# Kernel optimization log

Hardware: AMD Instinct MI355X
Metric: run time of the kernel (lower is better)

Reference implementation:

```python
import jax, jax.numpy as jnp
import numpy as np

B, TED, G, N, E, MD, NOISE = 10000, 512, 64, 2000, 64000, 15, 128
PAC = 10
PACDIM = (TED + NOISE) * PAC  # 6400
D0, D1 = 1024, 512


def _linear_params(k, fan_in, fan_out):
    kw, kb = jax.random.split(k)
    lim = 1.0 / np.sqrt(fan_in)
    w = jax.random.uniform(kw, (fan_in, fan_out), minval=-lim, maxval=lim, dtype=jnp.float32)
    b = jax.random.uniform(kb, (fan_out,), minval=-lim, maxval=lim, dtype=jnp.float32)
    return w, b


def setup_inputs() -> dict:
    key = jax.random.key(0)
    ks = jax.random.split(key, 12)
    inp = {
        'input_': jax.random.normal(ks[0], (B, TED), dtype=jnp.float32),
        'graphs_x': jax.random.normal(ks[1], (G, N, 1), dtype=jnp.float32),
        'edge_index': jax.random.randint(ks[2], (G, 2, E), 0, N, dtype=jnp.int32),
        'graph_ids': jax.random.randint(ks[3], (B,), 0, G, dtype=jnp.int32),
        'chain': jax.random.normal(ks[4], (B, 1), dtype=jnp.float32),
        'metadata': jax.random.normal(ks[5], (B, MD), dtype=jnp.float32),
    }
    inp['gcn_w'], inp['gcn_b'] = _linear_params(ks[6], 1, 1)
    inp['meta_w'], inp['meta_b'] = _linear_params(ks[7], 1 + MD, 32)
    inp['gme_w'], inp['gme_b'] = _linear_params(ks[8], N + 32, NOISE)
    inp['seq_w0'], inp['seq_b0'] = _linear_params(ks[9], PACDIM, D0)
    inp['seq_w1'], inp['seq_b1'] = _linear_params(ks[10], D0, D1)
    inp['seq_w2'], inp['seq_b2'] = _linear_params(ks[11], D1, 1)
    return inp


def _gcn_one(x, ei, gcn_w, gcn_b):
    # GCNConv(1,1) with self-loops and symmetric normalization.
    loops = jnp.arange(N, dtype=ei.dtype)
    src = jnp.concatenate([ei[0], loops])
    dst = jnp.concatenate([ei[1], loops])
    deg = jax.ops.segment_sum(jnp.ones_like(src, dtype=x.dtype), dst, num_segments=N)
    dinv = jax.lax.rsqrt(deg)  # deg >= 1 due to self-loops
    norm = dinv[src] * dinv[dst]  # [E+N]
    xw = x @ gcn_w  # [N,1]
    msg = xw[src] * norm[:, None]
    out = jax.ops.segment_sum(msg, dst, num_segments=N) + gcn_b
    return out.reshape(-1)  # flatten -> [N]


def reference(input_, graphs_x, edge_index, graph_ids, chain, metadata,
              gcn_w, gcn_b, meta_w, meta_b, gme_w, gme_b,
              seq_w0, seq_b0, seq_w1, seq_b1, seq_w2, seq_b2):
    # per-unique-graph GCN, vectorized over G graphs
    gcn_out = jax.vmap(lambda x, ei: _gcn_one(x, ei, gcn_w, gcn_b))(graphs_x, edge_index)  # [G,N]
    graph_emb = gcn_out[graph_ids]  # gather: [B,N]
    all_meta = jnp.concatenate([chain, metadata], axis=1)  # [B,1+MD]
    meta_emb = jax.nn.relu(all_meta @ meta_w + meta_b)  # [B,32]
    noise = jnp.concatenate([graph_emb, meta_emb], axis=1) @ gme_w + gme_b  # [B,NOISE]
    h = jnp.concatenate([input_, noise], axis=1).reshape(-1, PACDIM)  # [B/PAC, PACDIM]
    h = jax.nn.leaky_relu(h @ seq_w0 + seq_b0, 0.2)  # dropout omitted (eval mode)
    h = jax.nn.leaky_relu(h @ seq_w1 + seq_b1, 0.2)
    return h @ seq_w2 + seq_b2  # [B/PAC, 1]
```

## Files before the change

kernel.cpp:

```cpp
#include <hip/hip_runtime.h>

typedef __bf16 bf16_t;
typedef __bf16 bf16x4 __attribute__((ext_vector_type(4)));
typedef __bf16 bf16x8 __attribute__((ext_vector_type(8)));
typedef float floatx4 __attribute__((ext_vector_type(4)));

#define G_GRAPHS 64
#define N_NODES 2000
#define N_EDGES 64000
#define BATCH 10000
#define TED_ 512
#define NOISE_ 128
#define PACDIM_ 6400
#define D0_ 1024
#define D1_ 512
#define MROWS 1000
#define ESPLIT 8
#define EPB (N_EDGES / ESPLIT)
#define S0 8
#define S1 8

__device__ __forceinline__ void glds16(const void* g, void* l) {
    __builtin_amdgcn_global_load_lds(
        (__attribute__((address_space(1))) void*)(g),
        (__attribute__((address_space(3))) void*)(l), 16, 0, 0);
}

__global__ __launch_bounds__(256) void zero_kernel(float4* __restrict__ p, int n4) {
    int i = blockIdx.x * 256 + threadIdx.x;
    if (i < n4) p[i] = make_float4(0.f, 0.f, 0.f, 0.f);
}

__global__ __launch_bounds__(512) void deg_kernel(
    const int* __restrict__ edge_index, float* __restrict__ degs)
{
    __shared__ float h[N_NODES];
    const int g = blockIdx.y, s = blockIdx.x, tid = threadIdx.x;
    for (int n = tid; n < N_NODES; n += 512) h[n] = 0.f;
    __syncthreads();
    const int* dst = edge_index + (size_t)g * 2 * N_EDGES + N_EDGES + s * EPB;
    for (int e = tid; e < EPB; e += 512) atomicAdd(&h[dst[e]], 1.0f);
    __syncthreads();
    float* dg = degs + (size_t)g * N_NODES;
    for (int n = tid; n < N_NODES; n += 512) {
        float v = h[n];
        if (v != 0.f) atomicAdd(&dg[n], v);
    }
}

__global__ __launch_bounds__(512) void msg_kernel(
    const float* __restrict__ graphs_x, const int* __restrict__ edge_index,
    const float* __restrict__ degs, float* __restrict__ outs)
{
    __shared__ float xsl[N_NODES];
    __shared__ float dvl[N_NODES];
    __shared__ float oh[N_NODES];
    const int g = blockIdx.y, s = blockIdx.x, tid = threadIdx.x;
    const float* xg = graphs_x + (size_t)g * N_NODES;
    const float* dgg = degs + (size_t)g * N_NODES;
    for (int n = tid; n < N_NODES; n += 512) {
        xsl[n] = xg[n];
        dvl[n] = rsqrtf(dgg[n] + 1.0f);
        oh[n] = 0.f;
    }
    __syncthreads();
    const int* src = edge_index + (size_t)g * 2 * N_EDGES + s * EPB;
    const int* dst = src + N_EDGES;
    for (int e = tid; e < EPB; e += 512) {
        int ss = src[e], dd = dst[e];
        atomicAdd(&oh[dd], xsl[ss] * dvl[ss] * dvl[dd]);
    }
    __syncthreads();
    float* og = outs + (size_t)g * N_NODES;
    for (int n = tid; n < N_NODES; n += 512) {
        float v = oh[n];
        if (v != 0.f) atomicAdd(&og[n], v);
    }
}

__global__ __launch_bounds__(512) void gnoise_part_kernel(
    const float* __restrict__ graphs_x, const float* __restrict__ degs,
    const float* __restrict__ outs,
    const float* __restrict__ gcn_w, const float* __restrict__ gcn_b,
    const float* __restrict__ gme_w, float* __restrict__ gnoise)
{
    __shared__ float of[500];
    __shared__ float part[4][128];
    const int s = blockIdx.x, g = blockIdx.y, tid = threadIdx.x;
    const int nBase = s * 500;
    const float w = gcn_w[0], b = gcn_b[0];
    for (int n = tid; n < 500; n += 512) {
        int gn = nBase + n;
        float di2 = 1.0f / (degs[(size_t)g * N_NODES + gn] + 1.0f);
        of[n] = w * (outs[(size_t)g * N_NODES + gn]
                     + graphs_x[(size_t)g * N_NODES + gn] * di2) + b;
    }
    __syncthreads();
    const int j = tid & 127, ch = tid >> 7;
    float acc = 0.f;
    const int n0 = ch * 125;
    for (int n = n0; n < n0 + 125; n++)
        acc += of[n] * gme_w[(size_t)(nBase + n) * 128 + j];
    part[ch][j] = acc;
    __syncthreads();
    if (tid < 128)
        atomicAdd(&gnoise[(size_t)g * 128 + tid],
                  part[0][tid] + part[1][tid] + part[2][tid] + part[3][tid]);
}

__global__ __launch_bounds__(256) void pack_meta_kernel(
    const float* __restrict__ in,
    const float* __restrict__ chain, const float* __restrict__ metadata,
    const int* __restrict__ graph_ids,
    const float* __restrict__ meta_w, const float* __restrict__ meta_b,
    const float* __restrict__ gme_w, const float* __restrict__ gme_b,
    const float* __restrict__ gnoise, bf16_t* __restrict__ A)
{
    if (blockIdx.x < 5000) {
        int idx = blockIdx.x * 256 + threadIdx.x;
        float4 v = ((const float4*)in)[idx];
        int b = idx >> 7;
        int c = (idx & 127) << 2;
        int r = b / 10, slot = b - r * 10;
        bf16x4 o = { (bf16_t)v.x, (bf16_t)v.y, (bf16_t)v.z, (bf16_t)v.w };
        *(bf16x4*)(A + (size_t)r * PACDIM_ + slot * 640 + c) = o;
        return;
    }
    int wid = ((blockIdx.x - 5000) * 256 + threadIdx.x) >> 6;
    int lane = threadIdx.x & 63;
    if (wid >= BATCH) return;
    const int b = wid;
    float me = 0.f;
    if (lane < 32) {
        me = meta_b[lane] + chain[b] * meta_w[lane];
        for (int i = 1; i < 16; i++)
            me += metadata[(size_t)b * 15 + (i - 1)] * meta_w[(size_t)i * 32 + lane];
        me = me > 0.f ? me : 0.f;
    }
    const int gid = graph_ids[b];
    const int j1 = lane, j2 = lane + 64;
    float n1 = gnoise[(size_t)gid * 128 + j1] + gme_b[j1];
    float n2 = gnoise[(size_t)gid * 128 + j2] + gme_b[j2];
    for (int k = 0; k < 32; k++) {
        float mk = __shfl(me, k, 64);
        const float* wrow = gme_w + (size_t)(N_NODES + k) * 128;
        n1 += mk * wrow[j1];
        n2 += mk * wrow[j2];
    }
    int r = b / 10, slot = b - r * 10;
    bf16_t* dp = A + (size_t)r * PACDIM_ + slot * 640 + TED_;
    dp[j1] = (bf16_t)n1;
    dp[j2] = (bf16_t)n2;
}

__global__ __launch_bounds__(256) void transpose_bf16_kernel(
    const float* __restrict__ W, bf16_t* __restrict__ Wt, int R, int C)
{
    __shared__ float t[32][33];
    int c0 = blockIdx.x * 32, r0 = blockIdx.y * 32;
    int tx = threadIdx.x & 31, ty = threadIdx.x >> 5;
    for (int yy = ty; yy < 32; yy += 8)
        t[yy][tx] = W[(size_t)(r0 + yy) * C + c0 + tx];
    __syncthreads();
    for (int yy = ty; yy < 32; yy += 8)
        Wt[(size_t)(c0 + yy) * R + r0 + tx] = (bf16_t)t[tx][yy];
}

__global__ __launch_bounds__(256) void gemm_bt_splitk_kernel(
    const bf16_t* __restrict__ A,
    const bf16_t* __restrict__ Bt,
    float* __restrict__ P,
    int M, int N, int K, int KS)
{
    __shared__ __align__(16) bf16_t As[128 * 32];
    __shared__ __align__(16) bf16_t Bs[128 * 32];
    const int tid = threadIdx.x;
    const int wave = tid >> 6;
    const int lane = tid & 63;
    const int mBase = blockIdx.y * 128;
    const int nBase = blockIdx.x * 128;
    const int z = blockIdx.z;
    const int Mp = gridDim.y * 128;
    const int wm = (wave & 1) * 64;
    const int wn = (wave >> 1) * 64;

    floatx4 acc[4][4] = {};

    const int c0 = tid, c1 = tid + 256;
    const int rA0 = c0 >> 2, k80 = (c0 & 3) * 8;
    const int rA1 = c1 >> 2, k81 = (c1 & 3) * 8;
    int gm0 = mBase + rA0; if (gm0 > M - 1) gm0 = M - 1;
    int gm1 = mBase + rA1; if (gm1 > M - 1) gm1 = M - 1;
    const bf16_t* aP0 = A + (size_t)gm0 * K + k80;
    const bf16_t* aP1 = A + (size_t)gm1 * K + k81;
    const bf16_t* bP0 = Bt + (size_t)(nBase + rA0) * K + k80;
    const bf16_t* bP1 = Bt + (size_t)(nBase + rA1) * K + k81;
    char* lA0 = (char*)As + wave * 1024;
    char* lA1 = (char*)As + 4096 + wave * 1024;
    char* lB0 = (char*)Bs + wave * 1024;
    char* lB1 = (char*)Bs + 4096 + wave * 1024;

    const int kq = (lane >> 4) * 8;
    const int mr = lane & 15;
    const bf16x8* ra[4]; const bf16x8* rb[4];
    for (int i = 0; i < 4; i++)
        ra[i] = (const bf16x8*)&As[(wm + i * 16 + mr) * 32 + kq];
    for (int j = 0; j < 4; j++)
        rb[j] = (const bf16x8*)&Bs[(wn + j * 16 + mr) * 32 + kq];

    const int kEnd = z * KS + KS;
    for (int k0 = z * KS; k0 < kEnd; k0 += 32) {
        __syncthreads();
        glds16(aP0 + k0, lA0);
        glds16(aP1 + k0, lA1);
        glds16(bP0 + k0, lB0);
        glds16(bP1 + k0, lB1);
        __syncthreads();
        bf16x8 af[4], bfr[4];
        for (int i = 0; i < 4; i++) af[i] = *ra[i];
        for (int j = 0; j < 4; j++) bfr[j] = *rb[j];
        for (int i = 0; i < 4; i++)
            for (int j = 0; j < 4; j++)
                acc[i][j] = __builtin_amdgcn_mfma_f32_16x16x32_bf16(
                    af[i], bfr[j], acc[i][j], 0, 0, 0);
    }

    float* Pz = P + (size_t)z * Mp * N;
    const int rq = (lane >> 4) * 4;
    const int cn = lane & 15;
    for (int j = 0; j < 4; j++) {
        int col = nBase + wn + j * 16 + cn;
        for (int i = 0; i < 4; i++)
            for (int r = 0; r < 4; r++) {
                int rowm = mBase + wm + i * 16 + rq + r;
                Pz[(size_t)rowm * N + col] = acc[i][j][r];
            }
    }
}

__global__ __launch_bounds__(256) void reduce_bias_leaky_kernel(
    const float* __restrict__ P, const float* __restrict__ bias,
    bf16_t* __restrict__ C, int M, int N, int Mp, int S)
{
    int idx = blockIdx.x * 256 + threadIdx.x;
    int total = M * (N >> 2);
    if (idx >= total) return;
    int nv = N >> 2;
    int r = idx / nv, c4 = (idx - r * nv) << 2;
    size_t off = (size_t)r * N + c4;
    size_t stride = (size_t)Mp * N;
    float4 v = *(const float4*)(P + off);
    for (int s = 1; s < S; s++) {
        float4 u = *(const float4*)(P + s * stride + off);
        v.x += u.x; v.y += u.y; v.z += u.z; v.w += u.w;
    }
    const float4 bv = *(const float4*)(bias + c4);
    v.x += bv.x; v.y += bv.y; v.z += bv.z; v.w += bv.w;
    v.x = v.x > 0.f ? v.x : 0.2f * v.x;
    v.y = v.y > 0.f ? v.y : 0.2f * v.y;
    v.z = v.z > 0.f ? v.z : 0.2f * v.z;
    v.w = v.w > 0.f ? v.w : 0.2f * v.w;
    bf16x4 o = { (bf16_t)v.x, (bf16_t)v.y, (bf16_t)v.z, (bf16_t)v.w };
    *(bf16x4*)(C + off) = o;
}

__global__ __launch_bounds__(256) void final_fused_kernel(
    const float* __restrict__ P, const float* __restrict__ b1,
    const float* __restrict__ w2, const float* __restrict__ b2,
    float* __restrict__ out, int Mp, int S)
{
    int wid = (blockIdx.x * 256 + threadIdx.x) >> 6;
    int lane = threadIdx.x & 63;
    if (wid >= MROWS) return;
    size_t stride = (size_t)Mp * D1_;
    const float* base = P + (size_t)wid * D1_;
    float s = 0.f;
    for (int i = 0; i < 8; i++) {
        int c = i * 64 + lane;
        float v = base[c];
        for (int z = 1; z < S; z++) v += base[(size_t)z * stride + c];
        v += b1[c];
        v = v > 0.f ? v : 0.2f * v;
        s += v * w2[c];
    }
    for (int off = 32; off; off >>= 1) s += __shfl_down(s, off, 64);
    if (lane == 0) out[wid] = s + b2[0];
}

extern "C" void kernel_launch(void* const* d_in, const int* in_sizes, int n_in,
                              void* d_out, int out_size, void* d_ws, size_t ws_size,
                              hipStream_t stream)
{
    const float* input_    = (const float*)d_in[0];
    const float* graphs_x  = (const float*)d_in[1];
    const int*   edge_idx  = (const int*)  d_in[2];
    const int*   graph_ids = (const int*)  d_in[3];
    const float* chain     = (const float*)d_in[4];
    const float* metadata  = (const float*)d_in[5];
    const float* gcn_w     = (const float*)d_in[6];
    const float* gcn_b     = (const float*)d_in[7];
    const float* meta_w    = (const float*)d_in[8];
    const float* meta_b    = (const float*)d_in[9];
    const float* gme_w     = (const float*)d_in[10];
    const float* gme_b     = (const float*)d_in[11];
    const float* seq_w0    = (const float*)d_in[12];
    const float* seq_b0    = (const float*)d_in[13];
    const float* seq_w1    = (const float*)d_in[14];
    const float* seq_b1    = (const float*)d_in[15];
    const float* seq_w2    = (const float*)d_in[16];
    const float* seq_b2    = (const float*)d_in[17];
    float* out = (float*)d_out;

    char* ws = (char*)d_ws;
    float*  gnoise = (float*)(ws + 0);
    float*  degs   = (float*)(ws + 32768);
    float*  outs   = (float*)(ws + 544768);
    bf16_t* Abuf   = (bf16_t*)(ws + 1056768);
    bf16_t* W0t    = (bf16_t*)(ws + 13856768);
    bf16_t* W1t    = (bf16_t*)(ws + 26963968);
    bf16_t* H1     = (bf16_t*)(ws + 28012544);
    float*  P      = (float*)(ws + 30060544);

    const int zn4 = (32768 + 512000 + 512000) / 16;
    zero_kernel<<<(zn4 + 255) / 256, 256, 0, stream>>>((float4*)gnoise, zn4);
    deg_kernel<<<dim3(ESPLIT, G_GRAPHS), 512, 0, stream>>>(edge_idx, degs);
    msg_kernel<<<dim3(ESPLIT, G_GRAPHS), 512, 0, stream>>>(graphs_x, edge_idx, degs, outs);
    gnoise_part_kernel<<<dim3(4, G_GRAPHS), 512, 0, stream>>>(
        graphs_x, degs, outs, gcn_w, gcn_b, gme_w, gnoise);

    pack_meta_kernel<<<7500, 256, 0, stream>>>(
        input_, chain, metadata, graph_ids, meta_w, meta_b, gme_w, gme_b,
        gnoise, Abuf);
    transpose_bf16_kernel<<<dim3(D0_ / 32, PACDIM_ / 32), 256, 0, stream>>>(
        seq_w0, W0t, PACDIM_, D0_);
    transpose_bf16_kernel<<<dim3(D1_ / 32, D0_ / 32), 256, 0, stream>>>(
        seq_w1, W1t, D0_, D1_);

    gemm_bt_splitk_kernel<<<dim3(D0_ / 128, 8, S0), 256, 0, stream>>>(
        Abuf, W0t, P, MROWS, D0_, PACDIM_, PACDIM_ / S0);
    reduce_bias_leaky_kernel<<<(MROWS * D0_ / 4 + 255) / 256, 256, 0, stream>>>(
        P, seq_b0, H1, MROWS, D0_, 1024, S0);

    gemm_bt_splitk_kernel<<<dim3(D1_ / 128, 8, S1), 256, 0, stream>>>(
        H1, W1t, P, MROWS, D1_, D0_, D0_ / S1);
    final_fused_kernel<<<(MROWS * 64 + 255) / 256, 256, 0, stream>>>(
        P, seq_b1, seq_w2, seq_b2, out, 1024, S1);
}
```

Baseline: 279.0 us.

## Fuse prep kernels, replace global atomics with partial buffers, double-buffer GEMM LDS

Merges the degree histogram, input packing and both weight transposes into one prep kernel, which removes the zero kernel and several launches. Per-split degree and message results are now written to partial buffers and summed by the consumers instead of being accumulated with global atomics. The split-K GEMM gains double-buffered LDS so the next K tile loads while the current one is being multiplied, with one barrier per iteration. The cost is more workspace and extra partial-sum reads in the downstream kernels.

```diff
diff --git a/kernel.cpp b/kernel.cpp
--- a/kernel.cpp
+++ b/kernel.cpp
@@ -26,41 +26,69 @@
         (__attribute__((address_space(3))) void*)(l), 16, 0, 0);
 }
 
-__global__ __launch_bounds__(256) void zero_kernel(float4* __restrict__ p, int n4) {
-    int i = blockIdx.x * 256 + threadIdx.x;
-    if (i < n4) p[i] = make_float4(0.f, 0.f, 0.f, 0.f);
-}
-
-__global__ __launch_bounds__(512) void deg_kernel(
-    const int* __restrict__ edge_index, float* __restrict__ degs)
+__global__ __launch_bounds__(256) void prep_kernel(
+    const int* __restrict__ edge_index, float* __restrict__ degs_part,
+    const float* __restrict__ in, bf16_t* __restrict__ A,
+    const float* __restrict__ W0, bf16_t* __restrict__ W0t,
+    const float* __restrict__ W1, bf16_t* __restrict__ W1t)
 {
     __shared__ float h[N_NODES];
-    const int g = blockIdx.y, s = blockIdx.x, tid = threadIdx.x;
-    for (int n = tid; n < N_NODES; n += 512) h[n] = 0.f;
-    __syncthreads();
-    const int* dst = edge_index + (size_t)g * 2 * N_EDGES + N_EDGES + s * EPB;
-    for (int e = tid; e < EPB; e += 512) atomicAdd(&h[dst[e]], 1.0f);
-    __syncthreads();
-    float* dg = degs + (size_t)g * N_NODES;
-    for (int n = tid; n < N_NODES; n += 512) {
-        float v = h[n];
-        if (v != 0.f) atomicAdd(&dg[n], v);
-    }
+    __shared__ float t[32][33];
+    const int b = blockIdx.x, tid = threadIdx.x;
+    if (b < 512) {
+        const int s = b & 7, g = b >> 3;
+        for (int n = tid; n < N_NODES; n += 256) h[n] = 0.f;
+        __syncthreads();
+        const int* dst = edge_index + (size_t)g * 2 * N_EDGES + N_EDGES + s * EPB;
+        for (int e = tid; e < EPB; e += 256) atomicAdd(&h[dst[e]], 1.0f);
+        __syncthreads();
+        float* dp = degs_part + ((size_t)g * ESPLIT + s) * N_NODES;
+        for (int n = tid; n < N_NODES; n += 256) dp[n] = h[n];
+        return;
+    }
+    if (b < 5512) {
+        int idx = (b - 512) * 256 + tid;
+        float4 v = ((const float4*)in)[idx];
+        int bb = idx >> 7;
+        int c = (idx & 127) << 2;
+        int r = bb / 10, slot = bb - r * 10;
+        bf16x4 o = { (bf16_t)v.x, (bf16_t)v.y, (bf16_t)v.z, (bf16_t)v.w };
+        *(bf16x4*)(A + (size_t)r * PACDIM_ + slot * 640 + c) = o;
+        return;
+    }
+    const float* W; bf16_t* Wt; int Rr, Cc, c0, r0;
+    if (b < 11912) {
+        int tile = b - 5512;
+        W = W0; Wt = W0t; Rr = PACDIM_; Cc = D0_;
+        c0 = (tile & 31) << 5; r0 = (tile >> 5) << 5;
+    } else {
+        int tile = b - 11912;
+        W = W1; Wt = W1t; Rr = D0_; Cc = D1_;
+        c0 = (tile & 15) << 5; r0 = (tile >> 4) << 5;
+    }
+    int tx = tid & 31, ty = tid >> 5;
+    for (int yy = ty; yy < 32; yy += 8)
+        t[yy][tx] = W[(size_t)(r0 + yy) * Cc + c0 + tx];
+    __syncthreads();
+    for (int yy = ty; yy < 32; yy += 8)
+        Wt[(size_t)(c0 + yy) * Rr + r0 + tx] = (bf16_t)t[tx][yy];
 }
 
 __global__ __launch_bounds__(512) void msg_kernel(
     const float* __restrict__ graphs_x, const int* __restrict__ edge_index,
-    const float* __restrict__ degs, float* __restrict__ outs)
-{
-    __shared__ float xsl[N_NODES];
-    __shared__ float dvl[N_NODES];
+    const float* __restrict__ degs_part, float* __restrict__ outs_part)
+{
+    __shared__ float xs[N_NODES];
+    __shared__ float dv[N_NODES];
     __shared__ float oh[N_NODES];
     const int g = blockIdx.y, s = blockIdx.x, tid = threadIdx.x;
     const float* xg = graphs_x + (size_t)g * N_NODES;
-    const float* dgg = degs + (size_t)g * N_NODES;
+    const float* dgp = degs_part + (size_t)g * ESPLIT * N_NODES;
     for (int n = tid; n < N_NODES; n += 512) {
-        xsl[n] = xg[n];
-        dvl[n] = rsqrtf(dgg[n] + 1.0f);
+        xs[n] = xg[n];
+        float d = 1.0f;
+        for (int p = 0; p < ESPLIT; p++) d += dgp[(size_t)p * N_NODES + n];
+        dv[n] = rsqrtf(d);
         oh[n] = 0.f;
     }
     __syncthreads();
@@ -68,32 +96,34 @@
     const int* dst = src + N_EDGES;
     for (int e = tid; e < EPB; e += 512) {
         int ss = src[e], dd = dst[e];
-        atomicAdd(&oh[dd], xsl[ss] * dvl[ss] * dvl[dd]);
-    }
-    __syncthreads();
-    float* og = outs + (size_t)g * N_NODES;
-    for (int n = tid; n < N_NODES; n += 512) {
-        float v = oh[n];
-        if (v != 0.f) atomicAdd(&og[n], v);
-    }
-}
-
-__global__ __launch_bounds__(512) void gnoise_part_kernel(
-    const float* __restrict__ graphs_x, const float* __restrict__ degs,
-    const float* __restrict__ outs,
+        atomicAdd(&oh[dd], xs[ss] * dv[ss] * dv[dd]);
+    }
+    __syncthreads();
+    float* op = outs_part + ((size_t)g * ESPLIT + s) * N_NODES;
+    for (int n = tid; n < N_NODES; n += 512) op[n] = oh[n];
+}
+
+__global__ __launch_bounds__(512) void gnoise_kernel(
+    const float* __restrict__ graphs_x, const float* __restrict__ degs_part,
+    const float* __restrict__ outs_part,
     const float* __restrict__ gcn_w, const float* __restrict__ gcn_b,
-    const float* __restrict__ gme_w, float* __restrict__ gnoise)
+    const float* __restrict__ gme_w, float* __restrict__ gnoise_p)
 {
     __shared__ float of[500];
     __shared__ float part[4][128];
     const int s = blockIdx.x, g = blockIdx.y, tid = threadIdx.x;
     const int nBase = s * 500;
-    const float w = gcn_w[0], b = gcn_b[0];
+    const float w = gcn_w[0], bb = gcn_b[0];
+    const float* dgp = degs_part + (size_t)g * ESPLIT * N_NODES;
+    const float* otp = outs_part + (size_t)g * ESPLIT * N_NODES;
     for (int n = tid; n < 500; n += 512) {
         int gn = nBase + n;
-        float di2 = 1.0f / (degs[(size_t)g * N_NODES + gn] + 1.0f);
-        of[n] = w * (outs[(size_t)g * N_NODES + gn]
-                     + graphs_x[(size_t)g * N_NODES + gn] * di2) + b;
+        float d = 1.0f, o = 0.f;
+        for (int p = 0; p < ESPLIT; p++) {
+            d += dgp[(size_t)p * N_NODES + gn];
+            o += otp[(size_t)p * N_NODES + gn];
+        }
+        of[n] = w * (o + graphs_x[(size_t)g * N_NODES + gn] / d) + bb;
     }
     __syncthreads();
     const int j = tid & 127, ch = tid >> 7;
@@ -104,29 +134,18 @@
     part[ch][j] = acc;
     __syncthreads();
     if (tid < 128)
-        atomicAdd(&gnoise[(size_t)g * 128 + tid],
-                  part[0][tid] + part[1][tid] + part[2][tid] + part[3][tid]);
-}
-
-__global__ __launch_bounds__(256) void pack_meta_kernel(
-    const float* __restrict__ in,
+        gnoise_p[((size_t)g * 4 + s) * 128 + tid] =
+            part[0][tid] + part[1][tid] + part[2][tid] + part[3][tid];
+}
+
+__global__ __launch_bounds__(256) void meta_kernel(
     const float* __restrict__ chain, const float* __restrict__ metadata,
     const int* __restrict__ graph_ids,
     const float* __restrict__ meta_w, const float* __restrict__ meta_b,
     const float* __restrict__ gme_w, const float* __restrict__ gme_b,
-    const float* __restrict__ gnoise, bf16_t* __restrict__ A)
-{
-    if (blockIdx.x < 5000) {
-        int idx = blockIdx.x * 256 + threadIdx.x;
-        float4 v = ((const float4*)in)[idx];
-        int b = idx >> 7;
-        int c = (idx & 127) << 2;
-        int r = b / 10, slot = b - r * 10;
-        bf16x4 o = { (bf16_t)v.x, (bf16_t)v.y, (bf16_t)v.z, (bf16_t)v.w };
-        *(bf16x4*)(A + (size_t)r * PACDIM_ + slot * 640 + c) = o;
-        return;
-    }
-    int wid = ((blockIdx.x - 5000) * 256 + threadIdx.x) >> 6;
+    const float* __restrict__ gnoise_p, bf16_t* __restrict__ A)
+{
+    int wid = (blockIdx.x * 256 + threadIdx.x) >> 6;
     int lane = threadIdx.x & 63;
     if (wid >= BATCH) return;
     const int b = wid;
@@ -138,9 +157,10 @@
         me = me > 0.f ? me : 0.f;
     }
     const int gid = graph_ids[b];
+    const float* gp = gnoise_p + (size_t)gid * 4 * 128;
     const int j1 = lane, j2 = lane + 64;
-    float n1 = gnoise[(size_t)gid * 128 + j1] + gme_b[j1];
-    float n2 = gnoise[(size_t)gid * 128 + j2] + gme_b[j2];
+    float n1 = gme_b[j1] + gp[j1] + gp[128 + j1] + gp[256 + j1] + gp[384 + j1];
+    float n2 = gme_b[j2] + gp[j2] + gp[128 + j2] + gp[256 + j2] + gp[384 + j2];
     for (int k = 0; k < 32; k++) {
         float mk = __shfl(me, k, 64);
         const float* wrow = gme_w + (size_t)(N_NODES + k) * 128;
@@ -153,27 +173,14 @@
     dp[j2] = (bf16_t)n2;
 }
 
-__global__ __launch_bounds__(256) void transpose_bf16_kernel(
-    const float* __restrict__ W, bf16_t* __restrict__ Wt, int R, int C)
-{
-    __shared__ float t[32][33];
-    int c0 = blockIdx.x * 32, r0 = blockIdx.y * 32;
-    int tx = threadIdx.x & 31, ty = threadIdx.x >> 5;
-    for (int yy = ty; yy < 32; yy += 8)
-        t[yy][tx] = W[(size_t)(r0 + yy) * C + c0 + tx];
-    __syncthreads();
-    for (int yy = ty; yy < 32; yy += 8)
-        Wt[(size_t)(c0 + yy) * R + r0 + tx] = (bf16_t)t[tx][yy];
-}
-
 __global__ __launch_bounds__(256) void gemm_bt_splitk_kernel(
     const bf16_t* __restrict__ A,
     const bf16_t* __restrict__ Bt,
     float* __restrict__ P,
     int M, int N, int K, int KS)
 {
-    __shared__ __align__(16) bf16_t As[128 * 32];
-    __shared__ __align__(16) bf16_t Bs[128 * 32];
+    __shared__ __align__(16) bf16_t As[2][128 * 32];
+    __shared__ __align__(16) bf16_t Bs[2][128 * 32];
     const int tid = threadIdx.x;
     const int wave = tid >> 6;
     const int lane = tid & 63;
@@ -186,43 +193,52 @@
 
     floatx4 acc[4][4] = {};
 
-    const int c0 = tid, c1 = tid + 256;
-    const int rA0 = c0 >> 2, k80 = (c0 & 3) * 8;
-    const int rA1 = c1 >> 2, k81 = (c1 & 3) * 8;
-    int gm0 = mBase + rA0; if (gm0 > M - 1) gm0 = M - 1;
-    int gm1 = mBase + rA1; if (gm1 > M - 1) gm1 = M - 1;
+    const int rA0 = tid >> 2, k80 = (tid & 3) * 8;
+    int gm0 = mBase + rA0;      if (gm0 > M - 1) gm0 = M - 1;
+    int gm1 = mBase + 64 + rA0; if (gm1 > M - 1) gm1 = M - 1;
     const bf16_t* aP0 = A + (size_t)gm0 * K + k80;
-    const bf16_t* aP1 = A + (size_t)gm1 * K + k81;
+    const bf16_t* aP1 = A + (size_t)gm1 * K + k80;
     const bf16_t* bP0 = Bt + (size_t)(nBase + rA0) * K + k80;
-    const bf16_t* bP1 = Bt + (size_t)(nBase + rA1) * K + k81;
-    char* lA0 = (char*)As + wave * 1024;
-    char* lA1 = (char*)As + 4096 + wave * 1024;
-    char* lB0 = (char*)Bs + wave * 1024;
-    char* lB1 = (char*)Bs + 4096 + wave * 1024;
+    const bf16_t* bP1 = Bt + (size_t)(nBase + 64 + rA0) * K + k80;
 
     const int kq = (lane >> 4) * 8;
     const int mr = lane & 15;
-    const bf16x8* ra[4]; const bf16x8* rb[4];
-    for (int i = 0; i < 4; i++)
-        ra[i] = (const bf16x8*)&As[(wm + i * 16 + mr) * 32 + kq];
-    for (int j = 0; j < 4; j++)
-        rb[j] = (const bf16x8*)&Bs[(wn + j * 16 + mr) * 32 + kq];
-
-    const int kEnd = z * KS + KS;
-    for (int k0 = z * KS; k0 < kEnd; k0 += 32) {
-        __syncthreads();
-        glds16(aP0 + k0, lA0);
-        glds16(aP1 + k0, lA1);
-        glds16(bP0 + k0, lB0);
-        glds16(bP1 + k0, lB1);
-        __syncthreads();
+    int aOff[4], bOff[4];
+    for (int i = 0; i < 4; i++) aOff[i] = (wm + i * 16 + mr) * 32 + kq;
+    for (int j = 0; j < 4; j++) bOff[j] = (wn + j * 16 + mr) * 32 + kq;
+
+    const int nIter = KS >> 5;
+    const int kc = z * KS;
+    {
+        char* lA = (char*)(&As[0][0]) + wave * 1024;
+        char* lB = (char*)(&Bs[0][0]) + wave * 1024;
+        glds16(aP0 + kc, lA);
+        glds16(aP1 + kc, lA + 4096);
+        glds16(bP0 + kc, lB);
+        glds16(bP1 + kc, lB + 4096);
+    }
+    __syncthreads();
+    for (int t = 0; t < nIter; ++t) {
+        const int cur = t & 1;
+        if (t + 1 < nIter) {
+            const int kn = kc + (t + 1) * 32;
+            char* lA = (char*)(&As[cur ^ 1][0]) + wave * 1024;
+            char* lB = (char*)(&Bs[cur ^ 1][0]) + wave * 1024;
+            glds16(aP0 + kn, lA);
+            glds16(aP1 + kn, lA + 4096);
+            glds16(bP0 + kn, lB);
+            glds16(bP1 + kn, lB + 4096);
+        }
+        const bf16_t* aB = &As[cur][0];
+        const bf16_t* bB = &Bs[cur][0];
         bf16x8 af[4], bfr[4];
-        for (int i = 0; i < 4; i++) af[i] = *ra[i];
-        for (int j = 0; j < 4; j++) bfr[j] = *rb[j];
+        for (int i = 0; i < 4; i++) af[i] = *(const bf16x8*)(aB + aOff[i]);
+        for (int j = 0; j < 4; j++) bfr[j] = *(const bf16x8*)(bB + bOff[j]);
         for (int i = 0; i < 4; i++)
             for (int j = 0; j < 4; j++)
                 acc[i][j] = __builtin_amdgcn_mfma_f32_16x16x32_bf16(
                     af[i], bfr[j], acc[i][j], 0, 0, 0);
+        __syncthreads();
     }
 
     float* Pz = P + (size_t)z * Mp * N;
@@ -312,29 +328,24 @@
     float* out = (float*)d_out;
 
     char* ws = (char*)d_ws;
-    float*  gnoise = (float*)(ws + 0);
-    float*  degs   = (float*)(ws + 32768);
-    float*  outs   = (float*)(ws + 544768);
-    bf16_t* Abuf   = (bf16_t*)(ws + 1056768);
-    bf16_t* W0t    = (bf16_t*)(ws + 13856768);
-    bf16_t* W1t    = (bf16_t*)(ws + 26963968);
-    bf16_t* H1     = (bf16_t*)(ws + 28012544);
-    float*  P      = (float*)(ws + 30060544);
-
-    const int zn4 = (32768 + 512000 + 512000) / 16;
-    zero_kernel<<<(zn4 + 255) / 256, 256, 0, stream>>>((float4*)gnoise, zn4);
-    deg_kernel<<<dim3(ESPLIT, G_GRAPHS), 512, 0, stream>>>(edge_idx, degs);
-    msg_kernel<<<dim3(ESPLIT, G_GRAPHS), 512, 0, stream>>>(graphs_x, edge_idx, degs, outs);
-    gnoise_part_kernel<<<dim3(4, G_GRAPHS), 512, 0, stream>>>(
-        graphs_x, degs, outs, gcn_w, gcn_b, gme_w, gnoise);
-
-    pack_meta_kernel<<<7500, 256, 0, stream>>>(
-        input_, chain, metadata, graph_ids, meta_w, meta_b, gme_w, gme_b,
-        gnoise, Abuf);
-    transpose_bf16_kernel<<<dim3(D0_ / 32, PACDIM_ / 32), 256, 0, stream>>>(
-        seq_w0, W0t, PACDIM_, D0_);
-    transpose_bf16_kernel<<<dim3(D1_ / 32, D0_ / 32), 256, 0, stream>>>(
-        seq_w1, W1t, D0_, D1_);
+    float*  degs_part = (float*)(ws + 0);
+    float*  outs_part = (float*)(ws + 4096000);
+    float*  gnoise_p  = (float*)(ws + 8192000);
+    bf16_t* Abuf      = (bf16_t*)(ws + 8323072);
+    bf16_t* W0t       = (bf16_t*)(ws + 21123072);
+    bf16_t* W1t       = (bf16_t*)(ws + 34230272);
+    bf16_t* H1        = (bf16_t*)(ws + 35278848);
+    float*  P         = (float*)(ws + 37326848);
+
+    prep_kernel<<<12424, 256, 0, stream>>>(
+        edge_idx, degs_part, input_, Abuf, seq_w0, W0t, seq_w1, W1t);
+    msg_kernel<<<dim3(ESPLIT, G_GRAPHS), 512, 0, stream>>>(
+        graphs_x, edge_idx, degs_part, outs_part);
+    gnoise_kernel<<<dim3(4, G_GRAPHS), 512, 0, stream>>>(
+        graphs_x, degs_part, outs_part, gcn_w, gcn_b, gme_w, gnoise_p);
+    meta_kernel<<<2500, 256, 0, stream>>>(
+        chain, metadata, graph_ids, meta_w, meta_b, gme_w, gme_b,
+        gnoise_p, Abuf);
 
     gemm_bt_splitk_kernel<<<dim3(D0_ / 128, 8, S0), 256, 0, stream>>>(
         Abuf, W0t, P, MROWS, D0_, PACDIM_, PACDIM_ / S0);
```

Result: faster. 266.2 us (-4.6%).
